# Kernel optimization log

Measured on AMD Instinct MI355X. Metric: run time of the kernel, lower is better.

## Reference

```python
import jax, jax.numpy as jnp
import numpy as np

B, N, C = 4, 1370, 1024
H, DH = 16, C // 16
N_ROPE = 1369  # patch tokens covered by RoPE (prefix=1 CLS token)


def _rotate_half(x):
    x1, x2 = jnp.split(x, 2, axis=-1)
    return jnp.concatenate([-x2, x1], axis=-1)


def _rope_apply(x, sin, cos):
    return x * cos + _rotate_half(x) * sin


def setup_inputs() -> dict:
    key = jax.random.key(0)
    ks = jax.random.split(key, 7)
    return {
        "x": jax.random.normal(ks[0], (B, N, C), dtype=jnp.float32),
        "sin": jax.random.normal(ks[1], (N_ROPE, DH), dtype=jnp.float32),
        "cos": jax.random.normal(ks[2], (N_ROPE, DH), dtype=jnp.float32),
        "w_qkv": jax.random.normal(ks[3], (C, 3 * C), dtype=jnp.float32) * (C ** -0.5),
        "b_qkv": jax.random.normal(ks[4], (3 * C,), dtype=jnp.float32) * 0.02,
        "w_proj": jax.random.normal(ks[5], (C, C), dtype=jnp.float32) * (C ** -0.5),
        "b_proj": jax.random.normal(ks[6], (C,), dtype=jnp.float32) * 0.02,
    }


def reference(x, sin, cos, w_qkv, b_qkv, w_proj, b_proj):
    b, n, c = x.shape
    # QKV projection -> [3, B, H, N, DH]
    qkv = (x @ w_qkv + b_qkv).reshape(b, n, 3, H, DH).transpose(2, 0, 3, 1, 4)
    q, k, v = qkv[0], qkv[1], qkv[2]
    # RoPE on the last N_ROPE tokens (prefix tokens, e.g. CLS, left untouched)
    prefix = n - sin.shape[-2]
    q = jnp.concatenate([q[:, :, :prefix, :], _rope_apply(q[:, :, prefix:, :], sin, cos)], axis=-2)
    k = jnp.concatenate([k[:, :, :prefix, :], _rope_apply(k[:, :, prefix:, :], sin, cos)], axis=-2)
    # Full attention
    scale = 1.0 / jnp.sqrt(jnp.asarray(DH, dtype=x.dtype))
    attn = jnp.einsum('bhqd,bhkd->bhqk', q, k) * scale
    attn = jax.nn.softmax(attn, axis=-1)
    out = jnp.einsum('bhqk,bhkd->bhqd', attn, v)
    out = out.transpose(0, 2, 1, 3).reshape(b, n, c)
    return out @ w_proj + b_proj
```

## Files before the change

### kernel.cpp

```cpp
#include <hip/hip_runtime.h>
#include <hip/hip_bf16.h>

#define B_ 4
#define N_ 1370
#define C_ 1024
#define H_ 16
#define DH_ 64
#define NR_ 1369
#define M_ (B_*N_)
#define VTS_ 1408
#define ALS 64
#define PLS 72

#define QSCALE 0.1803368801111f

typedef _Float16 f16x8  __attribute__((ext_vector_type(8)));
typedef __bf16   bf16x8 __attribute__((ext_vector_type(8)));
typedef float    f32x4  __attribute__((ext_vector_type(4)));

__device__ __forceinline__ f16x8 ld_frag_h(const unsigned short* p) {
    uint4 u = *(const uint4*)p;
    return __builtin_bit_cast(f16x8, u);
}
__device__ __forceinline__ bf16x8 ld_frag_b(const unsigned short* p) {
    uint4 u = *(const uint4*)p;
    return __builtin_bit_cast(bf16x8, u);
}
__device__ __forceinline__ unsigned short f2h(float f) {
    _Float16 h = (_Float16)f;
    return __builtin_bit_cast(unsigned short, h);
}
__device__ __forceinline__ unsigned short f2bf(float f) {
    __hip_bfloat16 h = __float2bfloat16(f);
    return __builtin_bit_cast(unsigned short, h);
}
__device__ __forceinline__ bf16x8 ones_bf() {
    uint4 u = make_uint4(0x3F803F80u, 0x3F803F80u, 0x3F803F80u, 0x3F803F80u);
    return __builtin_bit_cast(bf16x8, u);
}

__device__ __forceinline__ void load_lds16(const unsigned short* g, unsigned short* l) {
    __builtin_amdgcn_global_load_lds(
        (const __attribute__((address_space(1))) unsigned int*)g,
        (__attribute__((address_space(3))) unsigned int*)l,
        16, 0, 0);
}

__global__ __launch_bounds__(256)
void conv_x_k(const float* __restrict__ x, unsigned short* __restrict__ xo, int total4) {
    int i = blockIdx.x * 256 + threadIdx.x;
    if (i >= total4) return;
    float4 v = ((const float4*)x)[i];
    ushort4 h;
    h.x = f2h(v.x); h.y = f2h(v.y); h.z = f2h(v.z); h.w = f2h(v.w);
    ((ushort4*)xo)[i] = h;
}

__global__ __launch_bounds__(256)
void conv_wt_k(const float* __restrict__ w, unsigned short* __restrict__ wt, int Ncol) {
    __shared__ unsigned short Th[64][68];
    const int tid = threadIdx.x, tx = tid & 15, ty = tid >> 4;
    const int k0 = blockIdx.y * 64, n0 = blockIdx.x * 64;
    #pragma unroll
    for (int i = 0; i < 4; ++i) {
        const int k = ty + i * 16;
        float4 v = *(const float4*)&w[(size_t)(k0 + k) * Ncol + n0 + tx * 4];
        Th[k][tx*4+0] = f2h(v.x); Th[k][tx*4+1] = f2h(v.y);
        Th[k][tx*4+2] = f2h(v.z); Th[k][tx*4+3] = f2h(v.w);
    }
    __syncthreads();
    #pragma unroll
    for (int i = 0; i < 4; ++i) {
        const int n = ty + i * 16;
        ushort4 o;
        o.x = Th[tx*4+0][n]; o.y = Th[tx*4+1][n]; o.z = Th[tx*4+2][n]; o.w = Th[tx*4+3][n];
        *(ushort4*)&wt[(size_t)(n0 + n) * 1024 + k0 + tx * 4] = o;
    }
}

__global__ __launch_bounds__(256)
void transpose_v_k(const unsigned short* __restrict__ v, unsigned short* __restrict__ vt) {
    __shared__ unsigned short Th[64][68];
    const int tid = threadIdx.x, tx = tid & 15, ty = tid >> 4;
    const int bh = blockIdx.y, t0 = blockIdx.x * 64;
    const unsigned short* vp = v + (size_t)bh * N_ * DH_;
    unsigned short* vtp = vt + (size_t)bh * DH_ * VTS_;
    #pragma unroll
    for (int i = 0; i < 4; ++i) {
        const int tok = ty + i * 16;
        const int gtok = t0 + tok;
        ushort4 val;
        if (gtok < N_) val = *(const ushort4*)&vp[(size_t)gtok * DH_ + tx * 4];
        else { val.x = 0; val.y = 0; val.z = 0; val.w = 0; }
        Th[tok][tx*4+0] = val.x; Th[tok][tx*4+1] = val.y;
        Th[tok][tx*4+2] = val.z; Th[tok][tx*4+3] = val.w;
    }
    __syncthreads();
    #pragma unroll
    for (int i = 0; i < 4; ++i) {
        const int d = ty + i * 16;
        ushort4 o;
        o.x = Th[tx*4+0][d]; o.y = Th[tx*4+1][d]; o.z = Th[tx*4+2][d]; o.w = Th[tx*4+3][d];
        *(ushort4*)&vtp[(size_t)d * VTS_ + t0 + tx * 4] = o;
    }
}

template<int MODE, int MT>
__global__ __launch_bounds__(256)
void gemm_mfma(const unsigned short* __restrict__ A, const unsigned short* __restrict__ Bt,
               const float* __restrict__ bias, float* __restrict__ out,
               unsigned short* __restrict__ qb, unsigned short* __restrict__ kb,
               unsigned short* __restrict__ vb,
               const float* __restrict__ sinp, const float* __restrict__ cosp,
               int nchunks)
{
    constexpr int MI = MT / 32;
    __shared__ __align__(16) unsigned short A_s[MT * 64];
    __shared__ __align__(16) unsigned short B_s[128 * 64];

    const int tid = threadIdx.x;
    const int wave = tid >> 6, lane = tid & 63;
    const int quad = lane >> 4, l16 = lane & 15;
    const int m0 = blockIdx.y * MT, n0 = blockIdx.x * 128;
    const int mwave = (wave & 1) * (MT / 2), nwave = (wave >> 1) * 64;

    const int srow = lane >> 3;
    const int gseg = (lane & 7) ^ srow;

    f32x4 acc[MI][4] = {};

    for (int kc = 0; kc < nchunks; ++kc) {
        const int kof = kc * 64;

        __syncthreads();
        #pragma unroll
        for (int i = 0; i < MI; ++i) {
            const int rbase = wave * (8 * MI) + i * 8;
            int arow = m0 + rbase + srow;
            if (arow > M_ - 1) arow = M_ - 1;
            load_lds16(A + (size_t)arow * 1024 + kof + gseg * 8, &A_s[rbase * 64]);
        }
        #pragma unroll
        for (int i = 0; i < 4; ++i) {
            const int rbase = wave * 32 + i * 8;
            const int brow = n0 + rbase + srow;
            load_lds16(Bt + (size_t)brow * 1024 + kof + gseg * 8, &B_s[rbase * 64]);
        }
        __syncthreads();

        #pragma unroll
        for (int kh = 0; kh < 2; ++kh) {
            const int soff = (((kh * 4 + quad) ^ (l16 & 7)) << 3);
            f16x8 a[MI], b[4];
            #pragma unroll
            for (int t = 0; t < MI; ++t)
                a[t] = ld_frag_h(&A_s[(mwave + t * 16 + l16) * 64 + soff]);
            #pragma unroll
            for (int t = 0; t < 4; ++t)
                b[t] = ld_frag_h(&B_s[(nwave + t * 16 + l16) * 64 + soff]);
            #pragma unroll
            for (int i = 0; i < MI; ++i)
                #pragma unroll
                for (int j = 0; j < 4; ++j)
                    acc[i][j] = __builtin_amdgcn_mfma_f32_16x16x32_f16(a[i], b[j], acc[i][j], 0, 0, 0);
        }
    }

    if (MODE == 0) {
        #pragma unroll
        for (int i = 0; i < MI; ++i) {
            #pragma unroll
            for (int r = 0; r < 4; ++r) {
                const int gm = m0 + mwave + i * 16 + quad * 4 + r;
                if (gm >= M_) continue;
                #pragma unroll
                for (int j = 0; j < 4; ++j) {
                    const int gn = n0 + nwave + j * 16 + l16;
                    out[(size_t)gm * 1024 + gn] = acc[i][j][r] + bias[gn];
                }
            }
        }
    } else {
        const int part = n0 >> 10;
        #pragma unroll
        for (int i = 0; i < MI; ++i) {
            #pragma unroll
            for (int r = 0; r < 4; ++r) {
                const int gm = m0 + mwave + i * 16 + quad * 4 + r;
                if (gm >= M_) continue;
                const int b = gm / N_;
                const int tok = gm - b * N_;

                float val[4];
                #pragma unroll
                for (int j = 0; j < 4; ++j) {
                    const int gn = n0 + nwave + j * 16 + l16;
                    val[j] = acc[i][j][r] + bias[gn];
                }

                if (part < 2 && tok >= 1) {
                    const float* sp = sinp + (size_t)(tok - 1) * DH_;
                    const float* cp = cosp + (size_t)(tok - 1) * DH_;
                    const float s0 = sp[l16],      s1 = sp[16 + l16];
                    const float s2 = sp[32 + l16], s3 = sp[48 + l16];
                    const float c0 = cp[l16],      c1 = cp[16 + l16];
                    const float c2 = cp[32 + l16], c3 = cp[48 + l16];
                    const float n0v = fmaf(val[0], c0, -val[2] * s0);
                    const float n1v = fmaf(val[1], c1, -val[3] * s1);
                    const float n2v = fmaf(val[2], c2,  val[0] * s2);
                    const float n3v = fmaf(val[3], c3,  val[1] * s3);
                    val[0] = n0v; val[1] = n1v; val[2] = n2v; val[3] = n3v;
                }

                #pragma unroll
                for (int j = 0; j < 4; ++j) {
                    const int gn = n0 + nwave + j * 16 + l16;
                    const int cc = gn & 1023;
                    const int h = cc >> 6, d = cc & 63;
                    const int bh = b * H_ + h;
                    if (part == 0)      qb[((size_t)bh * N_ + tok) * DH_ + d] = f2h(val[j] * QSCALE);
                    else if (part == 1) kb[((size_t)bh * N_ + tok) * DH_ + d] = f2h(val[j]);
                    else                vb[((size_t)bh * N_ + tok) * DH_ + d] = f2bf(val[j]);
                }
            }
        }
    }
}

__global__ __launch_bounds__(256)
void attn_k(const unsigned short* __restrict__ q, const unsigned short* __restrict__ k,
            const unsigned short* __restrict__ vt, unsigned short* __restrict__ out)
{
    __shared__ __align__(16) unsigned short Ks[2][64 * ALS];
    __shared__ __align__(16) unsigned short Vs[2][64 * ALS];
    __shared__ __align__(16) unsigned short Ps[4 * 32 * PLS];

    const int tid  = threadIdx.x;
    const int wave = tid >> 6, lane = tid & 63;
    const int quad = lane >> 4, l16 = lane & 15;
    const int srow = lane >> 3;
    const int gseg = (lane & 7) ^ srow;
    const int bh = blockIdx.y;
    const int q0 = blockIdx.x * 128;

    const unsigned short* qp  = q  + (size_t)bh * N_ * DH_;
    const unsigned short* kp  = k  + (size_t)bh * N_ * DH_;
    const unsigned short* vtp = vt + (size_t)bh * DH_ * VTS_;

    f16x8 qf[2][2];
    #pragma unroll
    for (int s = 0; s < 2; ++s) {
        int qrow = q0 + wave * 32 + s * 16 + l16;
        if (qrow > N_ - 1) qrow = N_ - 1;
        qf[s][0] = ld_frag_h(qp + (size_t)qrow * DH_ + quad * 8);
        qf[s][1] = ld_frag_h(qp + (size_t)qrow * DH_ + 32 + quad * 8);
    }

    const bf16x8 onesv = ones_bf();
    f32x4 O[2][4] = {};
    f32x4 L[2] = {};

    unsigned short* Pw = Ps + wave * 32 * PLS;
    const int so0 = ((quad)     ^ (l16 & 7)) << 3;
    const int so1 = ((4 + quad) ^ (l16 & 7)) << 3;

    auto stage = [&](int ch, int buf) {
        const int k0 = ch * 64;
        #pragma unroll
        for (int i = 0; i < 2; ++i) {
            const int rbase = wave * 16 + i * 8;
            int krow = k0 + rbase + srow;
            if (krow > N_ - 1) krow = N_ - 1;
            load_lds16(kp + (size_t)krow * DH_ + gseg * 8, &Ks[buf][rbase * ALS]);
            load_lds16(vtp + (size_t)(rbase + srow) * VTS_ + k0 + gseg * 8, &Vs[buf][rbase * ALS]);
        }
    };

    stage(0, 0);

    for (int ch = 0; ch < 22; ++ch) {
        const int k0 = ch * 64;
        const int cur = ch & 1;
        __syncthreads();
        if (ch + 1 < 22) stage(ch + 1, 1 - cur);

        f16x8 kf[4][2];
        #pragma unroll
        for (int t = 0; t < 4; ++t) {
            kf[t][0] = ld_frag_h(&Ks[cur][(t * 16 + l16) * ALS + so0]);
            kf[t][1] = ld_frag_h(&Ks[cur][(t * 16 + l16) * ALS + so1]);
        }
        f32x4 S[2][4];
        #pragma unroll
        for (int s = 0; s < 2; ++s) {
            #pragma unroll
            for (int t = 0; t < 4; ++t) {
                f32x4 z = {};
                z = __builtin_amdgcn_mfma_f32_16x16x32_f16(qf[s][0], kf[t][0], z, 0, 0, 0);
                z = __builtin_amdgcn_mfma_f32_16x16x32_f16(qf[s][1], kf[t][1], z, 0, 0, 0);
                S[s][t] = z;
            }
        }
        if (k0 + 64 > N_) {
            #pragma unroll
            for (int t = 0; t < 4; ++t) {
                if (k0 + t * 16 + l16 >= N_) {
                    #pragma unroll
                    for (int s = 0; s < 2; ++s) {
                        S[s][t][0] = -1e30f; S[s][t][1] = -1e30f;
                        S[s][t][2] = -1e30f; S[s][t][3] = -1e30f;
                    }
                }
            }
        }

        #pragma unroll
        for (int s = 0; s < 2; ++s) {
            #pragma unroll
            for (int t = 0; t < 4; ++t) {
                #pragma unroll
                for (int r = 0; r < 4; ++r) {
                    const float p = __builtin_amdgcn_exp2f(S[s][t][r]);
                    Pw[(s * 16 + quad * 4 + r) * PLS + t * 16 + l16] = f2bf(p);
                }
            }
        }
        __builtin_amdgcn_wave_barrier();

        bf16x8 pf[2][2];
        #pragma unroll
        for (int s = 0; s < 2; ++s) {
            pf[s][0] = ld_frag_b(&Pw[(s * 16 + l16) * PLS + quad * 8]);
            pf[s][1] = ld_frag_b(&Pw[(s * 16 + l16) * PLS + 32 + quad * 8]);
        }
        bf16x8 vf[4][2];
        #pragma unroll
        for (int dt = 0; dt < 4; ++dt) {
            vf[dt][0] = ld_frag_b(&Vs[cur][(dt * 16 + l16) * ALS + so0]);
            vf[dt][1] = ld_frag_b(&Vs[cur][(dt * 16 + l16) * ALS + so1]);
        }
        #pragma unroll
        for (int s = 0; s < 2; ++s) {
            L[s] = __builtin_amdgcn_mfma_f32_16x16x32_bf16(pf[s][0], onesv, L[s], 0, 0, 0);
            L[s] = __builtin_amdgcn_mfma_f32_16x16x32_bf16(pf[s][1], onesv, L[s], 0, 0, 0);
            #pragma unroll
            for (int dt = 0; dt < 4; ++dt) {
                O[s][dt] = __builtin_amdgcn_mfma_f32_16x16x32_bf16(pf[s][0], vf[dt][0], O[s][dt], 0, 0, 0);
                O[s][dt] = __builtin_amdgcn_mfma_f32_16x16x32_bf16(pf[s][1], vf[dt][1], O[s][dt], 0, 0, 0);
            }
        }
    }

    const int b = bh >> 4, h = bh & 15;
    #pragma unroll
    for (int s = 0; s < 2; ++s) {
        #pragma unroll
        for (int r = 0; r < 4; ++r) {
            const int qi = q0 + wave * 32 + s * 16 + quad * 4 + r;
            if (qi < N_) {
                const float inv = 1.0f / L[s][r];
                unsigned short* op = out + ((size_t)(b * N_ + qi)) * C_ + h * DH_ + l16;
                #pragma unroll
                for (int dt = 0; dt < 4; ++dt) op[dt * 16] = f2h(O[s][dt][r] * inv);
            }
        }
    }
}

extern "C" void kernel_launch(void* const* d_in, const int* in_sizes, int n_in,
                              void* d_out, int out_size, void* d_ws, size_t ws_size,
                              hipStream_t stream) {
    const float* x      = (const float*)d_in[0];
    const float* sinp   = (const float*)d_in[1];
    const float* cosp   = (const float*)d_in[2];
    const float* w_qkv  = (const float*)d_in[3];
    const float* b_qkv  = (const float*)d_in[4];
    const float* w_proj = (const float*)d_in[5];
    const float* b_proj = (const float*)d_in[6];
    float* out = (float*)d_out;

    unsigned short* p = (unsigned short*)d_ws;
    const size_t xsz  = (size_t)M_ * C_;
    const size_t wqsz = (size_t)3 * C_ * C_;
    const size_t wpsz = (size_t)C_ * C_;
    const size_t hsz  = (size_t)B_ * H_ * N_ * DH_;
    const size_t vtsz = (size_t)B_ * H_ * DH_ * VTS_;
    unsigned short* x_h   = p;            p += xsz;
    unsigned short* wq_t  = p;            p += wqsz;
    unsigned short* wp_t  = p;            p += wpsz;
    unsigned short* q     = p;            p += hsz;
    unsigned short* k     = p;            p += hsz;
    unsigned short* vt    = p;            p += vtsz;
    unsigned short* attnb = p;            p += xsz;
    unsigned short* vb    = attnb;

    conv_x_k<<<(int)((xsz / 4 + 255) / 256), 256, 0, stream>>>(x, x_h, (int)(xsz / 4));
    conv_wt_k<<<dim3(3 * C_ / 64, C_ / 64), 256, 0, stream>>>(w_qkv, wq_t, 3 * C_);
    conv_wt_k<<<dim3(C_ / 64, C_ / 64), 256, 0, stream>>>(w_proj, wp_t, C_);

    gemm_mfma<1, 128><<<dim3(3 * C_ / 128, (M_ + 127) / 128), 256, 0, stream>>>(
        x_h, wq_t, b_qkv, nullptr, q, k, vb, sinp, cosp, 16);

    transpose_v_k<<<dim3(VTS_ / 64, B_ * H_), 256, 0, stream>>>(vb, vt);

    attn_k<<<dim3((N_ + 127) / 128, B_ * H_), 256, 0, stream>>>(q, k, vt, attnb);

    gemm_mfma<0, 64><<<dim3(C_ / 128, (M_ + 63) / 64), 256, 0, stream>>>(
        attnb, wp_t, b_proj, out, nullptr, nullptr, nullptr, nullptr, nullptr, 16);
}
```

Baseline: 258.0 us.

## Add double-buffered 8-wave QKV GEMM kernel and MFMA priority hints in attention

Replaces the templated QKV projection with a dedicated 512-thread kernel using 192x128 tiles and double-buffered LDS staging, so the load of the next K chunk overlaps the MFMAs on the current one. The RoPE/scale/scatter epilogue is kept but simplified by hoisting part and head index per wave. The attention kernel gets s_setprio around its MFMA blocks to favour matrix issue over other waves. The larger LDS footprint (two 40 KB-ish buffers) may reduce occupancy, and the 192-row tile changes the grid shape and its tail handling.

New measurement: 255.0 us. Within noise of the previous version (-1.2%).

```diff
diff --git a/kernel.cpp b/kernel.cpp
--- a/kernel.cpp
+++ b/kernel.cpp
@@ -105,14 +105,117 @@
     }
 }
 
-template<int MODE, int MT>
+__global__ __launch_bounds__(512, 4)
+void gemm_qkv8(const unsigned short* __restrict__ A, const unsigned short* __restrict__ Bt,
+               const float* __restrict__ bias,
+               unsigned short* __restrict__ qb, unsigned short* __restrict__ kb,
+               unsigned short* __restrict__ vb,
+               const float* __restrict__ sinp, const float* __restrict__ cosp)
+{
+    __shared__ __align__(16) unsigned short A_s[2][192 * 64];
+    __shared__ __align__(16) unsigned short B_s[2][128 * 64];
+
+    const int tid = threadIdx.x;
+    const int wave = tid >> 6, lane = tid & 63;
+    const int quad = lane >> 4, l16 = lane & 15;
+    const int m0 = blockIdx.y * 192, n0 = blockIdx.x * 128;
+    const int mwave = (wave >> 1) * 48;
+    const int nwave = (wave & 1) * 64;
+
+    const int srow = lane >> 3;
+    const int gseg = (lane & 7) ^ srow;
+
+    f32x4 acc[3][4] = {};
+
+    auto stage = [&](int kc, int buf) {
+        const int kof = kc * 64;
+        #pragma unroll
+        for (int i = 0; i < 3; ++i) {
+            const int rbase = wave * 24 + i * 8;
+            int arow = m0 + rbase + srow;
+            if (arow > M_ - 1) arow = M_ - 1;
+            load_lds16(A + (size_t)arow * 1024 + kof + gseg * 8, &A_s[buf][rbase * 64]);
+        }
+        #pragma unroll
+        for (int i = 0; i < 2; ++i) {
+            const int rbase = wave * 16 + i * 8;
+            const int brow = n0 + rbase + srow;
+            load_lds16(Bt + (size_t)brow * 1024 + kof + gseg * 8, &B_s[buf][rbase * 64]);
+        }
+    };
+
+    stage(0, 0);
+
+    for (int kc = 0; kc < 16; ++kc) {
+        const int cur = kc & 1;
+        __syncthreads();
+        if (kc + 1 < 16) stage(kc + 1, cur ^ 1);
+
+        #pragma unroll
+        for (int kh = 0; kh < 2; ++kh) {
+            const int soff = (((kh * 4 + quad) ^ (l16 & 7)) << 3);
+            f16x8 a[3], b[4];
+            #pragma unroll
+            for (int t = 0; t < 3; ++t)
+                a[t] = ld_frag_h(&A_s[cur][(mwave + t * 16 + l16) * 64 + soff]);
+            #pragma unroll
+            for (int t = 0; t < 4; ++t)
+                b[t] = ld_frag_h(&B_s[cur][(nwave + t * 16 + l16) * 64 + soff]);
+            #pragma unroll
+            for (int i = 0; i < 3; ++i)
+                #pragma unroll
+                for (int j = 0; j < 4; ++j)
+                    acc[i][j] = __builtin_amdgcn_mfma_f32_16x16x32_f16(a[i], b[j], acc[i][j], 0, 0, 0);
+        }
+    }
+
+    const int nbase = n0 + nwave;
+    const int part = nbase >> 10;
+    const int h = (nbase & 1023) >> 6;
+    #pragma unroll
+    for (int i = 0; i < 3; ++i) {
+        #pragma unroll
+        for (int r = 0; r < 4; ++r) {
+            const int gm = m0 + mwave + i * 16 + quad * 4 + r;
+            if (gm >= M_) continue;
+            const int b = gm / N_;
+            const int tok = gm - b * N_;
+
+            float val[4];
+            #pragma unroll
+            for (int j = 0; j < 4; ++j)
+                val[j] = acc[i][j][r] + bias[nbase + j * 16 + l16];
+
+            if (part < 2 && tok >= 1) {
+                const float* sp = sinp + (size_t)(tok - 1) * DH_;
+                const float* cp = cosp + (size_t)(tok - 1) * DH_;
+                const float s0 = sp[l16],      s1 = sp[16 + l16];
+                const float s2 = sp[32 + l16], s3 = sp[48 + l16];
+                const float c0 = cp[l16],      c1 = cp[16 + l16];
+                const float c2 = cp[32 + l16], c3 = cp[48 + l16];
+                const float n0v = fmaf(val[0], c0, -val[2] * s0);
+                const float n1v = fmaf(val[1], c1, -val[3] * s1);
+                const float n2v = fmaf(val[2], c2,  val[0] * s2);
+                const float n3v = fmaf(val[3], c3,  val[1] * s3);
+                val[0] = n0v; val[1] = n1v; val[2] = n2v; val[3] = n3v;
+            }
+
+            const int bh = b * H_ + h;
+            #pragma unroll
+            for (int j = 0; j < 4; ++j) {
+                const int d = j * 16 + l16;
+                if (part == 0)      qb[((size_t)bh * N_ + tok) * DH_ + d] = f2h(val[j] * QSCALE);
+                else if (part == 1) kb[((size_t)bh * N_ + tok) * DH_ + d] = f2h(val[j]);
+                else                vb[((size_t)bh * N_ + tok) * DH_ + d] = f2bf(val[j]);
+            }
+        }
+    }
+}
+
+template<int MT>
 __global__ __launch_bounds__(256)
 void gemm_mfma(const unsigned short* __restrict__ A, const unsigned short* __restrict__ Bt,
-               const float* __restrict__ bias, float* __restrict__ out,
-               unsigned short* __restrict__ qb, unsigned short* __restrict__ kb,
-               unsigned short* __restrict__ vb,
-               const float* __restrict__ sinp, const float* __restrict__ cosp,
-               int nchunks)
+               const float* __restrict__ bias, float* __restrict__ out, int nchunks)
 {
     constexpr int MI = MT / 32;
     __shared__ __align__(16) unsigned short A_s[MT * 64];
@@ -166,62 +269,16 @@
         }
     }
 
-    if (MODE == 0) {
-        #pragma unroll
-        for (int i = 0; i < MI; ++i) {
-            #pragma unroll
-            for (int r = 0; r < 4; ++r) {
-                const int gm = m0 + mwave + i * 16 + quad * 4 + r;
-                if (gm >= M_) continue;
-                #pragma unroll
-                for (int j = 0; j < 4; ++j) {
-                    const int gn = n0 + nwave + j * 16 + l16;
-                    out[(size_t)gm * 1024 + gn] = acc[i][j][r] + bias[gn];
-                }
-            }
-        }
-    } else {
-        const int part = n0 >> 10;
-        #pragma unroll
-        for (int i = 0; i < MI; ++i) {
-            #pragma unroll
-            for (int r = 0; r < 4; ++r) {
-                const int gm = m0 + mwave + i * 16 + quad * 4 + r;
-                if (gm >= M_) continue;
-                const int b = gm / N_;
-                const int tok = gm - b * N_;
-
-                float val[4];
-                #pragma unroll
-                for (int j = 0; j < 4; ++j) {
-                    const int gn = n0 + nwave + j * 16 + l16;
-                    val[j] = acc[i][j][r] + bias[gn];
-                }
-
-                if (part < 2 && tok >= 1) {
-                    const float* sp = sinp + (size_t)(tok - 1) * DH_;
-                    const float* cp = cosp + (size_t)(tok - 1) * DH_;
-                    const float s0 = sp[l16],      s1 = sp[16 + l16];
-                    const float s2 = sp[32 + l16], s3 = sp[48 + l16];
-                    const float c0 = cp[l16],      c1 = cp[16 + l16];
-                    const float c2 = cp[32 + l16], c3 = cp[48 + l16];
-                    const float n0v = fmaf(val[0], c0, -val[2] * s0);
-                    const float n1v = fmaf(val[1], c1, -val[3] * s1);
-                    const float n2v = fmaf(val[2], c2,  val[0] * s2);
-                    const float n3v = fmaf(val[3], c3,  val[1] * s3);
-                    val[0] = n0v; val[1] = n1v; val[2] = n2v; val[3] = n3v;
-                }
-
-                #pragma unroll
-                for (int j = 0; j < 4; ++j) {
-                    const int gn = n0 + nwave + j * 16 + l16;
-                    const int cc = gn & 1023;
-                    const int h = cc >> 6, d = cc & 63;
-                    const int bh = b * H_ + h;
-                    if (part == 0)      qb[((size_t)bh * N_ + tok) * DH_ + d] = f2h(val[j] * QSCALE);
-                    else if (part == 1) kb[((size_t)bh * N_ + tok) * DH_ + d] = f2h(val[j]);
-                    else                vb[((size_t)bh * N_ + tok) * DH_ + d] = f2bf(val[j]);
-                }
+    #pragma unroll
+    for (int i = 0; i < MI; ++i) {
+        #pragma unroll
+        for (int r = 0; r < 4; ++r) {
+            const int gm = m0 + mwave + i * 16 + quad * 4 + r;
+            if (gm >= M_) continue;
+            #pragma unroll
+            for (int j = 0; j < 4; ++j) {
+                const int gn = n0 + nwave + j * 16 + l16;
+                out[(size_t)gm * 1024 + gn] = acc[i][j][r] + bias[gn];
             }
         }
     }
@@ -291,6 +348,7 @@
             kf[t][1] = ld_frag_h(&Ks[cur][(t * 16 + l16) * ALS + so1]);
         }
         f32x4 S[2][4];
+        __builtin_amdgcn_s_setprio(1);
         #pragma unroll
         for (int s = 0; s < 2; ++s) {
             #pragma unroll
@@ -301,6 +359,7 @@
                 S[s][t] = z;
             }
         }
+        __builtin_amdgcn_s_setprio(0);
         if (k0 + 64 > N_) {
             #pragma unroll
             for (int t = 0; t < 4; ++t) {
@@ -339,6 +398,7 @@
             vf[dt][0] = ld_frag_b(&Vs[cur][(dt * 16 + l16) * ALS + so0]);
             vf[dt][1] = ld_frag_b(&Vs[cur][(dt * 16 + l16) * ALS + so1]);
         }
+        __builtin_amdgcn_s_setprio(1);
         #pragma unroll
         for (int s = 0; s < 2; ++s) {
             L[s] = __builtin_amdgcn_mfma_f32_16x16x32_bf16(pf[s][0], onesv, L[s], 0, 0, 0);
@@ -349,6 +409,7 @@
                 O[s][dt] = __builtin_amdgcn_mfma_f32_16x16x32_bf16(pf[s][1], vf[dt][1], O[s][dt], 0, 0, 0);
             }
         }
+        __builtin_amdgcn_s_setprio(0);
     }
 
     const int b = bh >> 4, h = bh & 15;
@@ -398,13 +459,13 @@
     conv_wt_k<<<dim3(3 * C_ / 64, C_ / 64), 256, 0, stream>>>(w_qkv, wq_t, 3 * C_);
     conv_wt_k<<<dim3(C_ / 64, C_ / 64), 256, 0, stream>>>(w_proj, wp_t, C_);
 
-    gemm_mfma<1, 128><<<dim3(3 * C_ / 128, (M_ + 127) / 128), 256, 0, stream>>>(
-        x_h, wq_t, b_qkv, nullptr, q, k, vb, sinp, cosp, 16);
+    gemm_qkv8<<<dim3(3 * C_ / 128, (M_ + 191) / 192), 512, 0, stream>>>(
+        x_h, wq_t, b_qkv, q, k, vb, sinp, cosp);
 
     transpose_v_k<<<dim3(VTS_ / 64, B_ * H_), 256, 0, stream>>>(vb, vt);
 
     attn_k<<<dim3((N_ + 127) / 128, B_ * H_), 256, 0, stream>>>(q, k, vt, attnb);
 
-    gemm_mfma<0, 64><<<dim3(C_ / 128, (M_ + 63) / 64), 256, 0, stream>>>(
-        attnb, wp_t, b_proj, out, nullptr, nullptr, nullptr, nullptr, nullptr, 16);
-}
+    gemm_mfma<64><<<dim3(C_ / 128, (M_ + 63) / 64), 256, 0, stream>>>(
+        attnb, wp_t, b_proj, out, 16);
+}
```
